# Kernel tuning notes

Measured on AMD Instinct MI355X. Metric: run time of the kernel, lower is better.

## Reference

```python
import jax, jax.numpy as jnp
import numpy as np

N = 8192  # batch size
D = 256   # embedding dim


def setup_inputs() -> dict:
    key = jax.random.key(0)
    k1, k2 = jax.random.split(key)
    return {
        "embeddings": jax.random.normal(k1, (N, D), dtype=jnp.float32),
        "query_embeddings": jax.random.normal(k2, (N, D), dtype=jnp.float32),
    }


def _l2_normalize(x, eps=1e-8):
    # matches torch F.cosine_similarity: x / max(||x||, eps)
    n = jnp.sqrt(jnp.sum(x * x, axis=-1, keepdims=True))
    return x / jnp.maximum(n, eps)


def _cross_entropy(logits, targets):
    # mean CE; out-of-range targets clamp to last class (jit gather semantics)
    lse = jax.nn.logsumexp(logits, axis=1)
    t = jnp.clip(targets, 0, logits.shape[1] - 1)
    picked = jnp.take_along_axis(logits, t[:, None], axis=1)[:, 0]
    return jnp.mean(lse - picked)


def reference(embeddings, query_embeddings):
    n = embeddings.shape[0]
    # normalize once, then single NxN matmul (instead of NxNxD broadcast)
    sim = _l2_normalize(embeddings) @ _l2_normalize(query_embeddings).T  # (N, N)
    rows = jnp.arange(n)
    positives = jnp.diagonal(sim)[:, None]  # (N, 1)
    # off-diagonal gather: per row, column indices skipping the diagonal
    idx = jnp.arange(n - 1)
    cols = idx[None, :] + (idx[None, :] >= rows[:, None]).astype(jnp.int32)
    negatives = jnp.take_along_axis(sim, cols, axis=1)  # (N, N-1)
    loss_pos = _cross_entropy(positives, rows)
    loss_neg = _cross_entropy(-negatives, rows)
    return loss_pos + loss_neg
```

## Files before the change

### kernel.cpp

```cpp
#include <hip/hip_runtime.h>
#include <hip/hip_bf16.h>

#define NROWS 8192
#define DIM 256
#define NSPLIT 16
#define JSPAN (NROWS / NSPLIT)
#define TILE_COLS 64
#define TILE_BYTES (TILE_COLS * 512)
#define NT (JSPAN / TILE_COLS)
#define RPW 64
#define RPB 512
#define GRP_BYTES 8192

typedef __bf16 bf16x8 __attribute__((ext_vector_type(8)));
typedef float f32x4 __attribute__((ext_vector_type(4)));

#define NEG_LOG2E -1.4426950408889634f
#define NEG_LN2   -0.6931471805599453f

__global__ __launch_bounds__(256) void k_normalize_all(const float* __restrict__ emb,
                                                       const float* __restrict__ qry,
                                                       __hip_bfloat16* __restrict__ En,
                                                       __hip_bfloat16* __restrict__ Qn,
                                                       float* __restrict__ rowsum,
                                                       float* __restrict__ out) {
    if (blockIdx.x < 8)
        reinterpret_cast<float4*>(rowsum)[blockIdx.x * 256 + threadIdx.x] =
            float4{0.f, 0.f, 0.f, 0.f};
    if (blockIdx.x == 8 && threadIdx.x == 0) out[0] = 0.f;

    const int gr   = blockIdx.x * 4 + (threadIdx.x >> 6);
    const int lane = threadIdx.x & 63;
    const bool isE = (gr < NROWS);
    const float* in = isE ? emb : qry;
    const int row   = isE ? gr : gr - NROWS;
    const float scale = isE ? NEG_LOG2E : 1.0f;

    const float4 v = reinterpret_cast<const float4*>(in + (size_t)row * DIM)[lane];
    float ss = v.x * v.x + v.y * v.y + v.z * v.z + v.w * v.w;
#pragma unroll
    for (int m = 32; m >= 1; m >>= 1) ss += __shfl_xor(ss, m, 64);
    const float inv = scale / fmaxf(sqrtf(ss), 1e-8f);
    __hip_bfloat16 o[4];
    o[0] = __float2bfloat16(v.x * inv);
    o[1] = __float2bfloat16(v.y * inv);
    o[2] = __float2bfloat16(v.z * inv);
    o[3] = __float2bfloat16(v.w * inv);
    const ushort4 o8 = *reinterpret_cast<const ushort4*>(o);

    if (isE) {
        reinterpret_cast<ushort4*>(En + (size_t)row * DIM)[lane] = o8;
    } else {
        const int g = row >> 4, c = row & 15;
        char* dst = (char*)Qn + (size_t)g * GRP_BYTES
                    + (size_t)(lane >> 3) * 1024 + c * 64 + (lane & 7) * 8;
        *reinterpret_cast<ushort4*>(dst) = o8;
    }
}

__global__ __launch_bounds__(512, 2) void k_simlse(const __hip_bfloat16* __restrict__ En,
                                                   const __hip_bfloat16* __restrict__ Qn,
                                                   float* __restrict__ rowsum,
                                                   float* __restrict__ pickv) {
    __shared__ char lds[2][TILE_BYTES];
    const int bx   = blockIdx.x;
    const int ib   = bx >> 4;
    const int jq   = bx & 15;
    const int tid  = threadIdx.x;
    const int lane = tid & 63;
    const int w    = tid >> 6;
    const int l15  = lane & 15;
    const int lks  = lane >> 4;
    const int i0w  = ib * RPB + w * RPW;

    bf16x8 a[4][8];
    {
        const __hip_bfloat16* ab = En + (size_t)(i0w + l15) * DIM + lks * 8;
#pragma unroll
        for (int mi = 0; mi < 4; ++mi)
#pragma unroll
            for (int kk = 0; kk < 8; ++kk)
                a[mi][kk] = *reinterpret_cast<const bf16x8*>(ab + mi * 16 * DIM + kk * 32);
    }

    float racc[4][4];
#pragma unroll
    for (int mi = 0; mi < 4; ++mi)
#pragma unroll
        for (int r = 0; r < 4; ++r) racc[mi][r] = 0.0f;

    const int jq0 = jq * JSPAN;
    const char* qtile = (const char*)Qn + (size_t)jq0 * 512 + (size_t)lane * 16
                        + (size_t)w * 4096;

    auto stage_tile = [&](const char* src, char* buf) {
#pragma unroll
        for (int i = 0; i < 4; ++i)
            __builtin_amdgcn_global_load_lds(
                (const __attribute__((address_space(1))) void*)(src + i * 1024),
                (__attribute__((address_space(3))) void*)(buf + w * 4096 + i * 1024),
                16, 0, 0);
    };

    stage_tile(qtile, lds[0]);
    asm volatile("s_waitcnt vmcnt(0)" ::: "memory");
    __builtin_amdgcn_s_barrier();

    for (int t = 0; t < NT; ++t) {
        const char* cur = lds[t & 1];
        char* nxt       = lds[(t + 1) & 1];
        if (t + 1 < NT) stage_tile(qtile + TILE_BYTES, nxt);
        qtile += TILE_BYTES;

        const char* rd = cur + l15 * 64 + lks * 16;
        const int tbase = jq0 + t * TILE_COLS;

#pragma unroll
        for (int g = 0; g < 4; ++g) {
            bf16x8 b[8];
#pragma unroll
            for (int kk = 0; kk < 8; ++kk)
                b[kk] = *reinterpret_cast<const bf16x8*>(rd + (g * 8 + kk) * 1024);

            f32x4 acc[4];
#pragma unroll
            for (int mi = 0; mi < 4; ++mi) acc[mi] = f32x4{0.f, 0.f, 0.f, 0.f};

            __builtin_amdgcn_s_setprio(1);
#pragma unroll
            for (int kk = 0; kk < 8; ++kk)
#pragma unroll
                for (int mi = 0; mi < 4; ++mi)
                    acc[mi] = __builtin_amdgcn_mfma_f32_16x16x32_bf16(
                        a[mi][kk], b[kk], acc[mi], 0, 0, 0);
            __builtin_amdgcn_s_setprio(0);

            const int grpbase = tbase + g * 16;
            const bool spec = (grpbase <= i0w + RPW) && (grpbase + 16 > i0w);
            if (!spec) {
#pragma unroll
                for (int mi = 0; mi < 4; ++mi)
#pragma unroll
                    for (int r = 0; r < 4; ++r)
                        racc[mi][r] += __builtin_amdgcn_exp2f(acc[mi][r]);
            } else {
                const int jg = grpbase + l15;
#pragma unroll
                for (int mi = 0; mi < 4; ++mi) {
                    const int ig0 = i0w + mi * 16 + lks * 4;
#pragma unroll
                    for (int r = 0; r < 4; ++r) {
                        const float e  = __builtin_amdgcn_exp2f(acc[mi][r]);
                        const int   ig = ig0 + r;
                        racc[mi][r] += (jg == ig) ? 0.0f : e;
                        const int pc = (ig == NROWS - 1) ? (NROWS - 2) : (ig + 1);
                        if (jg == pc) pickv[ig] = acc[mi][r] * NEG_LN2;
                    }
                }
            }
        }

        if (t + 1 < NT) {
            asm volatile("s_waitcnt vmcnt(0)" ::: "memory");
            __builtin_amdgcn_s_barrier();
        }
    }

#pragma unroll
    for (int mi = 0; mi < 4; ++mi)
#pragma unroll
        for (int r = 0; r < 4; ++r) {
            float v = racc[mi][r];
            v += __shfl_xor(v, 1, 64);
            v += __shfl_xor(v, 2, 64);
            v += __shfl_xor(v, 4, 64);
            v += __shfl_xor(v, 8, 64);
            if (l15 == 0) atomicAdd(&rowsum[i0w + mi * 16 + lks * 4 + r], v);
        }
}

__global__ __launch_bounds__(256) void k_finalize(const float* __restrict__ rowsum,
                                                  const float* __restrict__ pickv,
                                                  float* __restrict__ out) {
    __shared__ float red[4];
    const int base = blockIdx.x * 512;
    float s = 0.0f;
#pragma unroll
    for (int it = 0; it < 2; ++it) {
        const int i = base + it * 256 + threadIdx.x;
        s += __logf(rowsum[i]) + pickv[i];
    }
#pragma unroll
    for (int m = 32; m >= 1; m >>= 1) s += __shfl_xor(s, m, 64);
    if ((threadIdx.x & 63) == 0) red[threadIdx.x >> 6] = s;
    __syncthreads();
    if (threadIdx.x == 0)
        atomicAdd(out, (red[0] + red[1] + red[2] + red[3]) * (1.0f / (float)NROWS));
}

extern "C" void kernel_launch(void* const* d_in, const int* in_sizes, int n_in,
                              void* d_out, int out_size, void* d_ws, size_t ws_size,
                              hipStream_t stream) {
    const float* emb = (const float*)d_in[0];
    const float* qry = (const float*)d_in[1];
    float* out = (float*)d_out;

    char* ws = (char*)d_ws;
    __hip_bfloat16* En = (__hip_bfloat16*)ws;
    __hip_bfloat16* Qn = (__hip_bfloat16*)(ws + (size_t)NROWS * DIM * 2);
    float* rowsum = (float*)(ws + (size_t)NROWS * DIM * 4);
    float* pickv  = rowsum + NROWS;

    k_normalize_all<<<2 * NROWS / 4, 256, 0, stream>>>(emb, qry, En, Qn, rowsum, out);
    k_simlse<<<16 * NSPLIT, 512, 0, stream>>>(En, Qn, rowsum, pickv);
    k_finalize<<<16, 256, 0, stream>>>(rowsum, pickv, out);
}
```

Measured before the change: 50.97 us.

## Triple-buffer Q tiles with per-chunk staging and finer-grained barriers

Changes the LDS pipeline in the similarity/LSE kernel from double to triple buffering, prefetching two tiles ahead. Each tile's load is split into four chunks issued between the MFMA groups, and partial vmcnt waits are used so loads overlap more with compute. It also hoists a per-tile diagonal check to skip the per-group special-case test. In exchange it uses 50% more LDS, which may limit the two-blocks-per-CU occupancy, and adds two barriers per group.

New measurement: 55.05 us. +8.0%, slower.

```diff
diff --git a/kernel.cpp b/kernel.cpp
--- a/kernel.cpp
+++ b/kernel.cpp
@@ -62,7 +62,7 @@
                                                    const __hip_bfloat16* __restrict__ Qn,
                                                    float* __restrict__ rowsum,
                                                    float* __restrict__ pickv) {
-    __shared__ char lds[2][TILE_BYTES];
+    __shared__ char lds[3][TILE_BYTES];
     const int bx   = blockIdx.x;
     const int ib   = bx >> 4;
     const int jq   = bx & 15;
@@ -90,30 +90,33 @@
         for (int r = 0; r < 4; ++r) racc[mi][r] = 0.0f;
 
     const int jq0 = jq * JSPAN;
-    const char* qtile = (const char*)Qn + (size_t)jq0 * 512 + (size_t)lane * 16
-                        + (size_t)w * 4096;
-
-    auto stage_tile = [&](const char* src, char* buf) {
-#pragma unroll
-        for (int i = 0; i < 4; ++i)
-            __builtin_amdgcn_global_load_lds(
-                (const __attribute__((address_space(1))) void*)(src + i * 1024),
-                (__attribute__((address_space(3))) void*)(buf + w * 4096 + i * 1024),
-                16, 0, 0);
+    const char* qsrc = (const char*)Qn + (size_t)jq0 * 512 + (size_t)lane * 16
+                       + (size_t)w * 4096;
+
+    auto stage_chunk = [&](int t, int g, char* buf) {
+        __builtin_amdgcn_global_load_lds(
+            (const __attribute__((address_space(1))) void*)
+                (qsrc + (size_t)t * TILE_BYTES + g * 1024),
+            (__attribute__((address_space(3))) void*)(buf + w * 4096 + g * 1024),
+            16, 0, 0);
     };
 
-    stage_tile(qtile, lds[0]);
-    asm volatile("s_waitcnt vmcnt(0)" ::: "memory");
+    char* b0 = lds[0];
+    char* b1 = lds[1];
+    char* b2 = lds[2];
+
+#pragma unroll
+    for (int g = 0; g < 4; ++g) stage_chunk(0, g, b0);
+#pragma unroll
+    for (int g = 0; g < 4; ++g) stage_chunk(1, g, b1);
+    asm volatile("s_waitcnt vmcnt(4)" ::: "memory");
+    __builtin_amdgcn_sched_barrier(0);
     __builtin_amdgcn_s_barrier();
 
     for (int t = 0; t < NT; ++t) {
-        const char* cur = lds[t & 1];
-        char* nxt       = lds[(t + 1) & 1];
-        if (t + 1 < NT) stage_tile(qtile + TILE_BYTES, nxt);
-        qtile += TILE_BYTES;
-
-        const char* rd = cur + l15 * 64 + lks * 16;
+        const char* rd = b0 + l15 * 64 + lks * 16;
         const int tbase = jq0 + t * TILE_COLS;
+        const bool spec_t = (tbase <= i0w + RPW) && (tbase + TILE_COLS > i0w);
 
 #pragma unroll
         for (int g = 0; g < 4; ++g) {
@@ -121,6 +124,12 @@
 #pragma unroll
             for (int kk = 0; kk < 8; ++kk)
                 b[kk] = *reinterpret_cast<const bf16x8*>(rd + (g * 8 + kk) * 1024);
+
+            if (t + 2 < NT) stage_chunk(t + 2, g, b2);
+
+            __builtin_amdgcn_s_barrier();
+            asm volatile("s_waitcnt lgkmcnt(0)" ::: "memory");
+            __builtin_amdgcn_sched_barrier(0);
 
             f32x4 acc[4];
 #pragma unroll
@@ -136,7 +145,7 @@
             __builtin_amdgcn_s_setprio(0);
 
             const int grpbase = tbase + g * 16;
-            const bool spec = (grpbase <= i0w + RPW) && (grpbase + 16 > i0w);
+            const bool spec = spec_t && (grpbase <= i0w + RPW) && (grpbase + 16 > i0w);
             if (!spec) {
 #pragma unroll
                 for (int mi = 0; mi < 4; ++mi)
@@ -158,12 +167,16 @@
                     }
                 }
             }
-        }
-
-        if (t + 1 < NT) {
-            asm volatile("s_waitcnt vmcnt(0)" ::: "memory");
+
+            if (g == 3 && t < NT - 1) {
+                if (t + 2 < NT) asm volatile("s_waitcnt vmcnt(4)" ::: "memory");
+                else            asm volatile("s_waitcnt vmcnt(0)" ::: "memory");
+                __builtin_amdgcn_sched_barrier(0);
+            }
             __builtin_amdgcn_s_barrier();
         }
+
+        char* tmp = b0; b0 = b1; b1 = b2; b2 = tmp;
     }
 
 #pragma unroll
```

## Switch similarity MFMA from 16x16x32 to 32x32x16 tiles with matching Q layout

Applied to the files above, without the earlier changes.

Replaces the 16x16x32 bf16 MFMA tiling with 32x32x16 MFMAs: each wave now holds two 32-row A tiles across 16 k-steps, and the Q operand is relaid out in 32-column groups so each B fragment is read straight from LDS. Larger MFMA tiles cut LDS B reads per FLOP and the number of instructions issued. The epilogue row-index mapping and the shuffle reduction change to match the 32x32 accumulator layout. The trade-off is different register pressure and a new layout whose indexing has to be exactly right.

Result: slower. 60.80 us (+19.3%).

```diff
diff --git a/kernel.cpp b/kernel.cpp
--- a/kernel.cpp
+++ b/kernel.cpp
@@ -10,10 +10,10 @@
 #define NT (JSPAN / TILE_COLS)
 #define RPW 64
 #define RPB 512
-#define GRP_BYTES 8192
+#define GRP32_BYTES 16384
 
 typedef __bf16 bf16x8 __attribute__((ext_vector_type(8)));
-typedef float f32x4 __attribute__((ext_vector_type(4)));
+typedef float f32x16 __attribute__((ext_vector_type(16)));
 
 #define NEG_LOG2E -1.4426950408889634f
 #define NEG_LN2   -0.6931471805599453f
@@ -51,9 +51,9 @@
     if (isE) {
         reinterpret_cast<ushort4*>(En + (size_t)row * DIM)[lane] = o8;
     } else {
-        const int g = row >> 4, c = row & 15;
-        char* dst = (char*)Qn + (size_t)g * GRP_BYTES
-                    + (size_t)(lane >> 3) * 1024 + c * 64 + (lane & 7) * 8;
+        const int g = row >> 5, c = row & 31;
+        char* dst = (char*)Qn + (size_t)g * GRP32_BYTES
+                    + (size_t)(lane >> 2) * 1024 + c * 32 + (lane & 3) * 8;
         *reinterpret_cast<ushort4*>(dst) = o8;
     }
 }
@@ -69,25 +69,25 @@
     const int tid  = threadIdx.x;
     const int lane = tid & 63;
     const int w    = tid >> 6;
-    const int l15  = lane & 15;
-    const int lks  = lane >> 4;
+    const int l31  = lane & 31;
+    const int hi   = lane >> 5;
     const int i0w  = ib * RPB + w * RPW;
 
-    bf16x8 a[4][8];
+    bf16x8 a[2][16];
     {
-        const __hip_bfloat16* ab = En + (size_t)(i0w + l15) * DIM + lks * 8;
-#pragma unroll
-        for (int mi = 0; mi < 4; ++mi)
-#pragma unroll
-            for (int kk = 0; kk < 8; ++kk)
-                a[mi][kk] = *reinterpret_cast<const bf16x8*>(ab + mi * 16 * DIM + kk * 32);
-    }
-
-    float racc[4][4];
-#pragma unroll
-    for (int mi = 0; mi < 4; ++mi)
-#pragma unroll
-        for (int r = 0; r < 4; ++r) racc[mi][r] = 0.0f;
+        const __hip_bfloat16* ab = En + (size_t)(i0w + l31) * DIM + hi * 8;
+#pragma unroll
+        for (int rt = 0; rt < 2; ++rt)
+#pragma unroll
+            for (int kk = 0; kk < 16; ++kk)
+                a[rt][kk] = *reinterpret_cast<const bf16x8*>(ab + rt * 32 * DIM + kk * 16);
+    }
+
+    float racc[2][16];
+#pragma unroll
+    for (int rt = 0; rt < 2; ++rt)
+#pragma unroll
+        for (int r = 0; r < 16; ++r) racc[rt][r] = 0.0f;
 
     const int jq0 = jq * JSPAN;
     const char* qtile = (const char*)Qn + (size_t)jq0 * 512 + (size_t)lane * 16
@@ -112,49 +112,44 @@
         if (t + 1 < NT) stage_tile(qtile + TILE_BYTES, nxt);
         qtile += TILE_BYTES;
 
-        const char* rd = cur + l15 * 64 + lks * 16;
+        const char* rd = cur + l31 * 32 + hi * 16;
         const int tbase = jq0 + t * TILE_COLS;
 
 #pragma unroll
-        for (int g = 0; g < 4; ++g) {
-            bf16x8 b[8];
-#pragma unroll
-            for (int kk = 0; kk < 8; ++kk)
-                b[kk] = *reinterpret_cast<const bf16x8*>(rd + (g * 8 + kk) * 1024);
-
-            f32x4 acc[4];
-#pragma unroll
-            for (int mi = 0; mi < 4; ++mi) acc[mi] = f32x4{0.f, 0.f, 0.f, 0.f};
+        for (int gg = 0; gg < 2; ++gg) {
+            f32x16 acc0 = {0.f}, acc1 = {0.f};
 
             __builtin_amdgcn_s_setprio(1);
 #pragma unroll
-            for (int kk = 0; kk < 8; ++kk)
-#pragma unroll
-                for (int mi = 0; mi < 4; ++mi)
-                    acc[mi] = __builtin_amdgcn_mfma_f32_16x16x32_bf16(
-                        a[mi][kk], b[kk], acc[mi], 0, 0, 0);
+            for (int kk = 0; kk < 16; ++kk) {
+                const bf16x8 b = *reinterpret_cast<const bf16x8*>(
+                    rd + gg * GRP32_BYTES + kk * 1024);
+                acc0 = __builtin_amdgcn_mfma_f32_32x32x16_bf16(a[0][kk], b, acc0, 0, 0, 0);
+                acc1 = __builtin_amdgcn_mfma_f32_32x32x16_bf16(a[1][kk], b, acc1, 0, 0, 0);
+            }
             __builtin_amdgcn_s_setprio(0);
 
-            const int grpbase = tbase + g * 16;
-            const bool spec = (grpbase <= i0w + RPW) && (grpbase + 16 > i0w);
+            const int grpbase = tbase + gg * 32;
+            const int jg = grpbase + l31;
+            const bool spec = (grpbase <= i0w + RPW) && (grpbase + 32 > i0w);
             if (!spec) {
 #pragma unroll
-                for (int mi = 0; mi < 4; ++mi)
-#pragma unroll
-                    for (int r = 0; r < 4; ++r)
-                        racc[mi][r] += __builtin_amdgcn_exp2f(acc[mi][r]);
+                for (int r = 0; r < 16; ++r) {
+                    racc[0][r] += __builtin_amdgcn_exp2f(acc0[r]);
+                    racc[1][r] += __builtin_amdgcn_exp2f(acc1[r]);
+                }
             } else {
-                const int jg = grpbase + l15;
-#pragma unroll
-                for (int mi = 0; mi < 4; ++mi) {
-                    const int ig0 = i0w + mi * 16 + lks * 4;
-#pragma unroll
-                    for (int r = 0; r < 4; ++r) {
-                        const float e  = __builtin_amdgcn_exp2f(acc[mi][r]);
-                        const int   ig = ig0 + r;
-                        racc[mi][r] += (jg == ig) ? 0.0f : e;
+#pragma unroll
+                for (int rt = 0; rt < 2; ++rt) {
+                    const int ig0 = i0w + rt * 32 + 4 * hi;
+#pragma unroll
+                    for (int r = 0; r < 16; ++r) {
+                        const float av = (rt == 0) ? acc0[r] : acc1[r];
+                        const float e  = __builtin_amdgcn_exp2f(av);
+                        const int   ig = ig0 + (r & 3) + 8 * (r >> 2);
+                        racc[rt][r] += (jg == ig) ? 0.0f : e;
                         const int pc = (ig == NROWS - 1) ? (NROWS - 2) : (ig + 1);
-                        if (jg == pc) pickv[ig] = acc[mi][r] * NEG_LN2;
+                        if (jg == pc) pickv[ig] = av * NEG_LN2;
                     }
                 }
             }
@@ -167,15 +162,17 @@
     }
 
 #pragma unroll
-    for (int mi = 0; mi < 4; ++mi)
-#pragma unroll
-        for (int r = 0; r < 4; ++r) {
-            float v = racc[mi][r];
+    for (int rt = 0; rt < 2; ++rt)
+#pragma unroll
+        for (int r = 0; r < 16; ++r) {
+            float v = racc[rt][r];
             v += __shfl_xor(v, 1, 64);
             v += __shfl_xor(v, 2, 64);
             v += __shfl_xor(v, 4, 64);
             v += __shfl_xor(v, 8, 64);
-            if (l15 == 0) atomicAdd(&rowsum[i0w + mi * 16 + lks * 4 + r], v);
+            v += __shfl_xor(v, 16, 64);
+            if (l31 == 0)
+                atomicAdd(&rowsum[i0w + rt * 32 + (r & 3) + 8 * (r >> 2) + 4 * hi], v);
         }
 }
 
```
